# Kernel optimization log

Measured on AMD Instinct MI355X. Metric: run time of the kernel, lower is better.

## Reference

```python
import jax, jax.numpy as jnp
import numpy as np

B, S, H = 4096, 256, 64


def setup_inputs() -> dict:
    key = jax.random.key(0)
    ks = jax.random.split(key, 9)
    s = 1.0 / np.sqrt(H)
    return {
        "x": jax.random.normal(ks[0], (B, S), jnp.float32),
        "W1": jax.random.normal(ks[1], (4, 1), jnp.float32),
        "b1": jax.random.normal(ks[2], (4,), jnp.float32) * 0.1,
        "W_ih": jax.random.normal(ks[3], (4 * H, 4), jnp.float32) * s,
        "W_hh": jax.random.normal(ks[4], (4 * H, H), jnp.float32) * s,
        "b_ih": jax.random.normal(ks[5], (4 * H,), jnp.float32) * s,
        "b_hh": jax.random.normal(ks[6], (4 * H,), jnp.float32) * s,
        "W2": jax.random.normal(ks[7], (1, H), jnp.float32) * s,
        "b2": jax.random.normal(ks[8], (1,), jnp.float32) * 0.1,
    }


def _lstm_last_h(fc1, W_ih, W_hh, b_ih, b_hh):
    # fc1: (B, S, 4). Precompute input contribution to gates for all steps.
    gx = jnp.einsum('bsi,gi->sbg', fc1, W_ih) + (b_ih + b_hh)  # (S, B, 4H)
    h0 = jnp.zeros((fc1.shape[0], H), fc1.dtype)
    c0 = jnp.zeros_like(h0)

    def step(carry, g_t):
        h, c = carry
        gates = g_t + h @ W_hh.T  # (B, 4H)
        i, f, g, o = jnp.split(gates, 4, axis=-1)  # PyTorch gate order i,f,g,o
        i = jax.nn.sigmoid(i)
        f = jax.nn.sigmoid(f)
        g = jnp.tanh(g)
        o = jax.nn.sigmoid(o)
        c = f * c + i * g
        h = o * jnp.tanh(c)
        return (h, c), None

    (h_last, _), _ = jax.lax.scan(step, (h0, c0), gx)
    return h_last  # (B, H)


def reference(x, W1, b1, W_ih, W_hh, b_ih, b_hh, W2, b2):
    # fc1: Linear(1->4) + tanh on x.unsqueeze(2)
    fc1 = jnp.tanh(x[..., None] * W1[:, 0] + b1)  # (B, S, 4)
    h_last = _lstm_last_h(fc1, W_ih, W_hh, b_ih, b_hh)
    return h_last @ W2.T + b2  # (B, 1)
```

## Files before the change

### kernel.cpp

```cpp
#include <hip/hip_runtime.h>


typedef __attribute__((ext_vector_type(8))) __bf16 bf16x8;
typedef __attribute__((ext_vector_type(4))) float f32x4;

#define S_LEN 256
#define TB 16
#define CHUNK 64
#define LOG2E 1.4426950408889634f

#if defined(__has_builtin) && __has_builtin(__builtin_amdgcn_exp2f)
#define EXP2F(x) __builtin_amdgcn_exp2f(x)
#else
#define EXP2F(x) exp2f(x)
#endif
#if defined(__has_builtin) && __has_builtin(__builtin_amdgcn_rcpf)
#define RCPF(x) __builtin_amdgcn_rcpf(x)
#else
#define RCPF(x) (1.0f / (x))
#endif

__device__ __forceinline__ float fast_tanh(float x) {
    float e = EXP2F(2.0f * LOG2E * x);
    return 1.0f - 2.0f * RCPF(e + 1.0f);
}

#define MFMA16(A, B, C) __builtin_amdgcn_mfma_f32_16x16x32_bf16((A), (B), (C), 0, 0, 0)

#define STEP(RB, WB, TLOC) do {                                                   \
    bf16x8 ah0 = *(const bf16x8*)&hbuf[RB][0][0][kg][col][0];                     \
    bf16x8 ah1 = *(const bf16x8*)&hbuf[RB][0][1][kg][col][0];                     \
    bf16x8 al0 = *(const bf16x8*)&hbuf[RB][1][0][kg][col][0];                     \
    bf16x8 al1 = *(const bf16x8*)&hbuf[RB][1][1][kg][col][0];                     \
    bf16x8 fa  = *(const bf16x8*)&fcfrag[TLOC][col][0];                           \
    if (kg >= 2) fa = zero8;                                                      \
    f32x4 acc[4];                                                                 \
    _Pragma("unroll")                                                             \
    for (int n = 0; n < 4; ++n) {                                                 \
        f32x4 a = MFMA16(fa,  whx[n],      biasq[n]);      \
        a       = MFMA16(ah0, whh_h[n][0], a);                                    \
        a       = MFMA16(ah1, whh_h[n][1], a);                                    \
        a       = MFMA16(al0, whh_h[n][0], a);                                    \
        a       = MFMA16(al1, whh_h[n][1], a);                                    \
        a       = MFMA16(ah0, whh_l[n][0], a);                                    \
        a       = MFMA16(ah1, whh_l[n][1], a);                                    \
        acc[n] = a;                                                               \
    }                                                                             \
    _Pragma("unroll")                                                             \
    for (int r = 0; r < 4; ++r) {                                                 \
                        \
        float ei = EXP2F(-acc[0][r]); float iv = RCPF(1.0f + ei);                 \
        float ef = EXP2F(-acc[1][r]); float fv = RCPF(1.0f + ef);                 \
        float eg = EXP2F( acc[2][r]); float gv = 1.0f - 2.0f * RCPF(1.0f + eg);   \
        float eo = EXP2F(-acc[3][r]); float ov = RCPF(1.0f + eo);                 \
        float cv = fv * cst[r] + iv * gv; cst[r] = cv;                            \
        float ec = EXP2F((2.0f * LOG2E) * cv);                                    \
        float th = 1.0f - 2.0f * RCPF(1.0f + ec);                                 \
        float hv = ov * th; hlast[r] = hv;                                        \
        __bf16 hi = (__bf16)hv; __bf16 lo = (__bf16)(hv - (float)hi);             \
        hbuf[WB][0][uks][ukg][kg * 4 + r][up] = hi;                               \
        hbuf[WB][1][uks][ukg][kg * 4 + r][up] = lo;                               \
    }                                                                             \
    __syncthreads();                                                              \
} while (0)

__global__ __launch_bounds__(256, 1)
void lstm_fused(const float* __restrict__ x,
                const float* __restrict__ W1, const float* __restrict__ b1,
                const float* __restrict__ W_ih, const float* __restrict__ W_hh,
                const float* __restrict__ b_ih, const float* __restrict__ b_hh,
                const float* __restrict__ W2, const float* __restrict__ b2,
                float* __restrict__ out)
{
    __shared__ __bf16 fcfrag[CHUNK][TB][8];
    __shared__ __bf16 hbuf[2][2][2][4][TB][8];
    __shared__ float hfin[64][TB];

    const int tid  = threadIdx.x;
    const int lane = tid & 63;
    const int wv   = tid >> 6;
    const int col  = lane & 15;
    const int kg   = lane >> 4;
    const int b0   = blockIdx.x * TB;

    bf16x8 whh_h[4][2], whh_l[4][2];
    bf16x8 whx[4];
    f32x4  biasq[4];

    bf16x8 zero8;
    #pragma unroll
    for (int j = 0; j < 8; ++j) zero8[j] = (__bf16)0.0f;

    #pragma unroll
    for (int n = 0; n < 4; ++n) {
        const int g = 16 * (wv + 4 * n) + col;
        const float sc = (n == 2) ? (2.0f * LOG2E) : LOG2E;
        #pragma unroll
        for (int ks = 0; ks < 2; ++ks) {
            const float* wp = &W_hh[g * 64 + ks * 32 + kg * 8];
            #pragma unroll
            for (int j = 0; j < 8; ++j) {
                float wf  = sc * wp[j];
                __bf16 hi = (__bf16)wf;
                whh_h[n][ks][j] = hi;
                whh_l[n][ks][j] = (__bf16)(wf - (float)hi);
            }
        }
        whx[n] = zero8;
        if (kg < 2) {
            #pragma unroll
            for (int j = 0; j < 4; ++j) {
                float wf  = sc * W_ih[g * 4 + j];
                __bf16 hi = (__bf16)wf;
                __bf16 v  = (kg == 0) ? hi : (__bf16)(wf - (float)hi);
                whx[n][j] = v; whx[n][j + 4] = v;
            }
        }
        const float bs = sc * (b_ih[g] + b_hh[g]);
        biasq[n][0] = bs; biasq[n][1] = bs; biasq[n][2] = bs; biasq[n][3] = bs;
    }

    {
        f32x4 zv = {0.f, 0.f, 0.f, 0.f};
        ((f32x4*)&hbuf[0][0][0][0][0][0])[tid] = zv;
    }

    float w1r[4], b1r[4];
    #pragma unroll
    for (int j = 0; j < 4; ++j) { w1r[j] = W1[j]; b1r[j] = b1[j]; }

    float cst[4] = {0.f, 0.f, 0.f, 0.f};
    float hlast[4];

    const int u   = 16 * wv + col;
    const int uks = u >> 5, ukg = (u >> 3) & 3, up = u & 7;

    for (int t = 0; t < S_LEN; t += 2) {
        if ((t & (CHUNK - 1)) == 0) {
            __syncthreads();
            const int rr = tid & 15;
            const int tq = tid >> 4;
            f32x4 xv = *(const f32x4*)&x[(b0 + rr) * S_LEN + t + tq * 4];
            #pragma unroll
            for (int tl = 0; tl < 4; ++tl) {
                bf16x8 v;
                #pragma unroll
                for (int j = 0; j < 4; ++j) {
                    float fc  = fast_tanh(xv[tl] * w1r[j] + b1r[j]);
                    __bf16 hi = (__bf16)fc;
                    v[j]     = hi;
                    v[j + 4] = (__bf16)(fc - (float)hi);
                }
                *(bf16x8*)&fcfrag[tq * 4 + tl][rr][0] = v;
            }
            __syncthreads();
        }
        STEP(0, 1, (t & (CHUNK - 1)));
        STEP(1, 0, ((t + 1) & (CHUNK - 1)));
    }

    #pragma unroll
    for (int r = 0; r < 4; ++r) hfin[u][kg * 4 + r] = hlast[r];
    __syncthreads();
    if (tid < TB) {
        float s = b2[0];
        #pragma unroll
        for (int uu = 0; uu < 64; ++uu) s += hfin[uu][tid] * W2[uu];
        out[b0 + tid] = s;
    }
}

extern "C" void kernel_launch(void* const* d_in, const int* in_sizes, int n_in,
                              void* d_out, int out_size, void* d_ws, size_t ws_size,
                              hipStream_t stream) {
    (void)in_sizes; (void)n_in; (void)d_ws; (void)ws_size; (void)out_size;
    const float* x    = (const float*)d_in[0];
    const float* W1   = (const float*)d_in[1];
    const float* b1   = (const float*)d_in[2];
    const float* W_ih = (const float*)d_in[3];
    const float* W_hh = (const float*)d_in[4];
    const float* b_ih = (const float*)d_in[5];
    const float* b_hh = (const float*)d_in[6];
    const float* W2   = (const float*)d_in[7];
    const float* b2   = (const float*)d_in[8];
    float* out = (float*)d_out;
    lstm_fused<<<4096 / TB, 256, 0, stream>>>(x, W1, b1, W_ih, W_hh, b_ih, b_hh, W2, b2, out);
}
```

Measured before the change: 230.5 us.

## Split batch tile across two wave groups and pack hi/lo h into MFMA K dimension

Doubles the block to 512 threads, with two wave groups each handling 8 of the 16 batch rows. The A operand now packs the hi and lo bf16 halves of h along the MFMA K lanes, so each gate tile takes 5 MFMAs instead of 7. The two K halves are summed with a cross-lane shuffle, which also halves the per-lane activation work. This cuts the serial per-step MFMA chain and the transcendental count per wave, at the cost of extra shuffles, a larger block and twice the waves sharing each barrier.

```diff
diff --git a/kernel.cpp b/kernel.cpp
--- a/kernel.cpp
+++ b/kernel.cpp
@@ -3,6 +3,7 @@
 
 typedef __attribute__((ext_vector_type(8))) __bf16 bf16x8;
 typedef __attribute__((ext_vector_type(4))) float f32x4;
+typedef __attribute__((ext_vector_type(2))) float f32x2;
 
 #define S_LEN 256
 #define TB 16
@@ -27,44 +28,52 @@
 
 #define MFMA16(A, B, C) __builtin_amdgcn_mfma_f32_16x16x32_bf16((A), (B), (C), 0, 0, 0)
 
-#define STEP(RB, WB, TLOC) do {                                                   \
-    bf16x8 ah0 = *(const bf16x8*)&hbuf[RB][0][0][kg][col][0];                     \
-    bf16x8 ah1 = *(const bf16x8*)&hbuf[RB][0][1][kg][col][0];                     \
-    bf16x8 al0 = *(const bf16x8*)&hbuf[RB][1][0][kg][col][0];                     \
-    bf16x8 al1 = *(const bf16x8*)&hbuf[RB][1][1][kg][col][0];                     \
-    bf16x8 fa  = *(const bf16x8*)&fcfrag[TLOC][col][0];                           \
-    if (kg >= 2) fa = zero8;                                                      \
-    f32x4 acc[4];                                                                 \
-    _Pragma("unroll")                                                             \
-    for (int n = 0; n < 4; ++n) {                                                 \
-        f32x4 a = MFMA16(fa,  whx[n],      biasq[n]);      \
-        a       = MFMA16(ah0, whh_h[n][0], a);                                    \
-        a       = MFMA16(ah1, whh_h[n][1], a);                                    \
-        a       = MFMA16(al0, whh_h[n][0], a);                                    \
-        a       = MFMA16(al1, whh_h[n][1], a);                                    \
-        a       = MFMA16(ah0, whh_l[n][0], a);                                    \
-        a       = MFMA16(ah1, whh_l[n][1], a);                                    \
-        acc[n] = a;                                                               \
-    }                                                                             \
-    _Pragma("unroll")                                                             \
-    for (int r = 0; r < 4; ++r) {                                                 \
-                        \
-        float ei = EXP2F(-acc[0][r]); float iv = RCPF(1.0f + ei);                 \
-        float ef = EXP2F(-acc[1][r]); float fv = RCPF(1.0f + ef);                 \
-        float eg = EXP2F( acc[2][r]); float gv = 1.0f - 2.0f * RCPF(1.0f + eg);   \
-        float eo = EXP2F(-acc[3][r]); float ov = RCPF(1.0f + eo);                 \
-        float cv = fv * cst[r] + iv * gv; cst[r] = cv;                            \
-        float ec = EXP2F((2.0f * LOG2E) * cv);                                    \
-        float th = 1.0f - 2.0f * RCPF(1.0f + ec);                                 \
-        float hv = ov * th; hlast[r] = hv;                                        \
-        __bf16 hi = (__bf16)hv; __bf16 lo = (__bf16)(hv - (float)hi);             \
-        hbuf[WB][0][uks][ukg][kg * 4 + r][up] = hi;                               \
-        hbuf[WB][1][uks][ukg][kg * 4 + r][up] = lo;                               \
-    }                                                                             \
-    __syncthreads();                                                              \
+#define STEP(RB, WB, TLOC) do {                                                  \
+    bf16x8 ap0 = *(const bf16x8*)&hbuf[hv][RB][ahl][0][kg][arow][0];             \
+    bf16x8 ap1 = *(const bf16x8*)&hbuf[hv][RB][ahl][1][kg][arow][0];             \
+    bf16x8 fa  = *(const bf16x8*)&fcfrag[TLOC][farow][0];                        \
+    if (col >= 8) fa = zero8;                 \
+    f32x4 acc[4];                                                                \
+    _Pragma("unroll")                                                            \
+    for (int n = 0; n < 4; ++n) {                                                \
+        f32x4 a = MFMA16(fa,  whx[n],      biasq[n]);    \
+        a       = MFMA16(ap0, whh_h[n][0], a);       \
+        a       = MFMA16(ap1, whh_h[n][1], a);                          \
+        a       = MFMA16(ap0, whh_l[n][0], a);       \
+        a       = MFMA16(ap1, whh_l[n][1], a);                          \
+        acc[n] = a;                                                              \
+    }                                                                            \
+         \
+          \
+    float gate[4][2];                                                            \
+    _Pragma("unroll")                                                            \
+    for (int n = 0; n < 4; ++n) {                                                \
+        float own0 = upper ? acc[n][2] : acc[n][0];                              \
+        float own1 = upper ? acc[n][3] : acc[n][1];                              \
+        float snd0 = upper ? acc[n][0] : acc[n][2];                              \
+        float snd1 = upper ? acc[n][1] : acc[n][3];                              \
+        gate[n][0] = own0 + __shfl_xor(snd0, 32);                                \
+        gate[n][1] = own1 + __shfl_xor(snd1, 32);                                \
+    }                                                                            \
+    _Pragma("unroll")                                                            \
+    for (int r = 0; r < 2; ++r) {                                                \
+                           \
+        float ei = EXP2F(-gate[0][r]); float iv = RCPF(1.0f + ei);               \
+        float ef = EXP2F(-gate[1][r]); float fv = RCPF(1.0f + ef);               \
+        float eg = EXP2F( gate[2][r]); float gv = 1.0f - 2.0f * RCPF(1.0f + eg); \
+        float eo = EXP2F(-gate[3][r]); float ov = RCPF(1.0f + eo);               \
+        float cv = fv * cst[r] + iv * gv; cst[r] = cv;                           \
+        float ec = EXP2F((2.0f * LOG2E) * cv);                                   \
+        float th = 1.0f - 2.0f * RCPF(1.0f + ec);                                \
+        float hvv = ov * th; hlast[r] = hvv;                                     \
+        __bf16 hh = (__bf16)hvv; __bf16 hl = (__bf16)(hvv - (float)hh);          \
+        hbuf[hv][WB][0][uks][ukg][row_base + r][up] = hh;                        \
+        hbuf[hv][WB][1][uks][ukg][row_base + r][up] = hl;                        \
+    }                                                                            \
+    __syncthreads();                                                             \
 } while (0)
 
-__global__ __launch_bounds__(256, 1)
+__global__ __launch_bounds__(512, 1)
 void lstm_fused(const float* __restrict__ x,
                 const float* __restrict__ W1, const float* __restrict__ b1,
                 const float* __restrict__ W_ih, const float* __restrict__ W_hh,
@@ -73,27 +82,37 @@
                 float* __restrict__ out)
 {
     __shared__ __bf16 fcfrag[CHUNK][TB][8];
-    __shared__ __bf16 hbuf[2][2][2][4][TB][8];
+    __shared__ __bf16 hbuf[2][2][2][2][4][8][8];
     __shared__ float hfin[64][TB];
 
     const int tid  = threadIdx.x;
     const int lane = tid & 63;
-    const int wv   = tid >> 6;
+    const int wv8  = tid >> 6;
+    const int hv   = wv8 >> 2;
+    const int wl   = wv8 & 3;
     const int col  = lane & 15;
     const int kg   = lane >> 4;
     const int b0   = blockIdx.x * TB;
 
+    const int  ahl   = col >> 3;
+    const int  arow  = col & 7;
+    const int  farow = 8 * hv + (col & 7);
+    const bool upper = (kg >= 2);
+    const int  row_base = (kg & 1) * 4 + (kg >> 1) * 2;
+    const int  u   = 16 * wl + col;
+    const int  uks = u >> 5, ukg = (u >> 3) & 3, up = u & 7;
+
+    bf16x8 zero8;
+    #pragma unroll
+    for (int j = 0; j < 8; ++j) zero8[j] = (__bf16)0.0f;
+
     bf16x8 whh_h[4][2], whh_l[4][2];
     bf16x8 whx[4];
     f32x4  biasq[4];
 
-    bf16x8 zero8;
-    #pragma unroll
-    for (int j = 0; j < 8; ++j) zero8[j] = (__bf16)0.0f;
-
     #pragma unroll
     for (int n = 0; n < 4; ++n) {
-        const int g = 16 * (wv + 4 * n) + col;
+        const int g = 16 * (wl + 4 * n) + col;
         const float sc = (n == 2) ? (2.0f * LOG2E) : LOG2E;
         #pragma unroll
         for (int ks = 0; ks < 2; ++ks) {
@@ -116,33 +135,30 @@
                 whx[n][j] = v; whx[n][j + 4] = v;
             }
         }
-        const float bs = sc * (b_ih[g] + b_hh[g]);
+        const float bs = (kg < 2) ? sc * (b_ih[g] + b_hh[g]) : 0.0f;
         biasq[n][0] = bs; biasq[n][1] = bs; biasq[n][2] = bs; biasq[n][3] = bs;
     }
 
     {
         f32x4 zv = {0.f, 0.f, 0.f, 0.f};
-        ((f32x4*)&hbuf[0][0][0][0][0][0])[tid] = zv;
+        ((f32x4*)&hbuf[0][0][0][0][0][0][0])[tid] = zv;
     }
 
     float w1r[4], b1r[4];
     #pragma unroll
     for (int j = 0; j < 4; ++j) { w1r[j] = W1[j]; b1r[j] = b1[j]; }
 
-    float cst[4] = {0.f, 0.f, 0.f, 0.f};
-    float hlast[4];
-
-    const int u   = 16 * wv + col;
-    const int uks = u >> 5, ukg = (u >> 3) & 3, up = u & 7;
+    f32x2 cst = {0.f, 0.f};
+    float hlast[2];
 
     for (int t = 0; t < S_LEN; t += 2) {
         if ((t & (CHUNK - 1)) == 0) {
             __syncthreads();
             const int rr = tid & 15;
             const int tq = tid >> 4;
-            f32x4 xv = *(const f32x4*)&x[(b0 + rr) * S_LEN + t + tq * 4];
+            f32x2 xv = *(const f32x2*)&x[(b0 + rr) * S_LEN + t + tq * 2];
             #pragma unroll
-            for (int tl = 0; tl < 4; ++tl) {
+            for (int tl = 0; tl < 2; ++tl) {
                 bf16x8 v;
                 #pragma unroll
                 for (int j = 0; j < 4; ++j) {
@@ -151,7 +167,7 @@
                     v[j]     = hi;
                     v[j + 4] = (__bf16)(fc - (float)hi);
                 }
-                *(bf16x8*)&fcfrag[tq * 4 + tl][rr][0] = v;
+                *(bf16x8*)&fcfrag[tq * 2 + tl][rr][0] = v;
             }
             __syncthreads();
         }
@@ -159,8 +175,8 @@
         STEP(1, 0, ((t + 1) & (CHUNK - 1)));
     }
 
-    #pragma unroll
-    for (int r = 0; r < 4; ++r) hfin[u][kg * 4 + r] = hlast[r];
+    hfin[u][8 * hv + row_base + 0] = hlast[0];
+    hfin[u][8 * hv + row_base + 1] = hlast[1];
     __syncthreads();
     if (tid < TB) {
         float s = b2[0];
@@ -184,5 +200,5 @@
     const float* W2   = (const float*)d_in[7];
     const float* b2   = (const float*)d_in[8];
     float* out = (float*)d_out;
-    lstm_fused<<<4096 / TB, 256, 0, stream>>>(x, W1, b1, W_ih, W_hh, b_ih, b_hh, W2, b2, out);
+    lstm_fused<<<4096 / TB, 512, 0, stream>>>(x, W1, b1, W_ih, W_hh, b_ih, b_hh, W2, b2, out);
 }
```

Measured after the change: 269.2 us. +16.8%, slower.

## Pack hi/lo bf16 split into MFMA K dimension with 8-row blocks

Applied to the files above, without the earlier changes.

Halves the batch tile per block to 8 rows and re-lays out the hidden-state buffer so each MFMA row pair holds the hi and lo bf16 halves of one batch row. The split-precision product then comes out of 4 MFMAs per gate instead of 6, with the two partial sums added after the MFMA. The gate math is also rewritten to fuse the sigmoid and tanh reciprocals into fewer RCP calls, with clamping to avoid overflow. Launch bounds now allow two blocks per CU to make up for the smaller tiles. The catch is twice as many blocks, each doing the same per-step sync and MFMA latency chain on half the useful rows.

```diff
diff --git a/kernel.cpp b/kernel.cpp
--- a/kernel.cpp
+++ b/kernel.cpp
@@ -3,11 +3,13 @@
 
 typedef __attribute__((ext_vector_type(8))) __bf16 bf16x8;
 typedef __attribute__((ext_vector_type(4))) float f32x4;
+typedef __attribute__((ext_vector_type(2))) float f32x2;
 
 #define S_LEN 256
-#define TB 16
+#define TB 8
 #define CHUNK 64
 #define LOG2E 1.4426950408889634f
+#define TWO_LOG2E 2.8853900817779268f
 
 #if defined(__has_builtin) && __has_builtin(__builtin_amdgcn_exp2f)
 #define EXP2F(x) __builtin_amdgcn_exp2f(x)
@@ -20,51 +22,55 @@
 #define RCPF(x) (1.0f / (x))
 #endif
 
+__device__ __forceinline__ float clamp30(float x) {
+    return fminf(fmaxf(x, -30.0f), 30.0f);
+}
 __device__ __forceinline__ float fast_tanh(float x) {
-    float e = EXP2F(2.0f * LOG2E * x);
+    float e = EXP2F(TWO_LOG2E * x);
     return 1.0f - 2.0f * RCPF(e + 1.0f);
 }
 
 #define MFMA16(A, B, C) __builtin_amdgcn_mfma_f32_16x16x32_bf16((A), (B), (C), 0, 0, 0)
 
 #define STEP(RB, WB, TLOC) do {                                                   \
-    bf16x8 ah0 = *(const bf16x8*)&hbuf[RB][0][0][kg][col][0];                     \
-    bf16x8 ah1 = *(const bf16x8*)&hbuf[RB][0][1][kg][col][0];                     \
-    bf16x8 al0 = *(const bf16x8*)&hbuf[RB][1][0][kg][col][0];                     \
-    bf16x8 al1 = *(const bf16x8*)&hbuf[RB][1][1][kg][col][0];                     \
-    bf16x8 fa  = *(const bf16x8*)&fcfrag[TLOC][col][0];                           \
-    if (kg >= 2) fa = zero8;                                                      \
+    bf16x8 ap0 = *(const bf16x8*)&hbuf[RB][0][kg][col >> 1][col & 1][0];          \
+    bf16x8 ap1 = *(const bf16x8*)&hbuf[RB][1][kg][col >> 1][col & 1][0];          \
+    bf16x8 fa  = *(const bf16x8*)&fcfrag[TLOC][col >> 1][0];                      \
+    if (col & 1) fa = zero8;                \
     f32x4 acc[4];                                                                 \
     _Pragma("unroll")                                                             \
     for (int n = 0; n < 4; ++n) {                                                 \
-        f32x4 a = MFMA16(fa,  whx[n],      biasq[n]);      \
-        a       = MFMA16(ah0, whh_h[n][0], a);                                    \
-        a       = MFMA16(ah1, whh_h[n][1], a);                                    \
-        a       = MFMA16(al0, whh_h[n][0], a);                                    \
-        a       = MFMA16(al1, whh_h[n][1], a);                                    \
-        a       = MFMA16(ah0, whh_l[n][0], a);                                    \
-        a       = MFMA16(ah1, whh_l[n][1], a);                                    \
+        f32x4 a = MFMA16(fa,  whx[n],      biasq[n]);     \
+        a       = MFMA16(ap0, whh_h[n][0], a);                                    \
+        a       = MFMA16(ap1, whh_h[n][1], a);                                    \
+        a       = MFMA16(ap0, whh_l[n][0], a);                                    \
+        a       = MFMA16(ap1, whh_l[n][1], a);                                    \
         acc[n] = a;                                                               \
     }                                                                             \
     _Pragma("unroll")                                                             \
-    for (int r = 0; r < 4; ++r) {                                                 \
-                        \
-        float ei = EXP2F(-acc[0][r]); float iv = RCPF(1.0f + ei);                 \
-        float ef = EXP2F(-acc[1][r]); float fv = RCPF(1.0f + ef);                 \
-        float eg = EXP2F( acc[2][r]); float gv = 1.0f - 2.0f * RCPF(1.0f + eg);   \
-        float eo = EXP2F(-acc[3][r]); float ov = RCPF(1.0f + eo);                 \
-        float cv = fv * cst[r] + iv * gv; cst[r] = cv;                            \
-        float ec = EXP2F((2.0f * LOG2E) * cv);                                    \
-        float th = 1.0f - 2.0f * RCPF(1.0f + ec);                                 \
-        float hv = ov * th; hlast[r] = hv;                                        \
-        __bf16 hi = (__bf16)hv; __bf16 lo = (__bf16)(hv - (float)hi);             \
-        hbuf[WB][0][uks][ukg][kg * 4 + r][up] = hi;                               \
-        hbuf[WB][1][uks][ukg][kg * 4 + r][up] = lo;                               \
+    for (int j = 0; j < 2; ++j) {                                                 \
+            \
+        float Ai = clamp30(acc[0][2 * j] + acc[0][2 * j + 1]);                    \
+        float Ff = clamp30(acc[1][2 * j] + acc[1][2 * j + 1]);                    \
+        float Gg = clamp30(acc[2][2 * j] + acc[2][2 * j + 1]);                    \
+        float Oo = clamp30(acc[3][2 * j] + acc[3][2 * j + 1]);                    \
+        float ea = EXP2F(-Ai), ef = EXP2F(-Ff), eg = EXP2F(Gg), eo = EXP2F(-Oo);  \
+        float tf  = 1.0f + ef;                                                    \
+        float tag = (1.0f + ea) * (1.0f + eg);                                    \
+        float Nn  = fmaf(cst[j], tag, (eg - 1.0f) * tf);                          \
+        float cn  = Nn * RCPF(tag * tf);                                          \
+        cst[j] = cn;                                                              \
+        float ec  = EXP2F(clamp30(TWO_LOG2E * cn));                               \
+        float hvv = (ec - 1.0f) * RCPF((1.0f + eo) * (ec + 1.0f));                \
+        hlast[j] = hvv;                                                           \
+        __bf16 hh = (__bf16)hvv; __bf16 hl = (__bf16)(hvv - (float)hh);           \
+        hbuf[WB][uks][ukg][2 * kg + j][0][up] = hh;                               \
+        hbuf[WB][uks][ukg][2 * kg + j][1][up] = hl;                               \
     }                                                                             \
     __syncthreads();                                                              \
 } while (0)
 
-__global__ __launch_bounds__(256, 1)
+__global__ __launch_bounds__(256, 2)
 void lstm_fused(const float* __restrict__ x,
                 const float* __restrict__ W1, const float* __restrict__ b1,
                 const float* __restrict__ W_ih, const float* __restrict__ W_hh,
@@ -73,7 +79,7 @@
                 float* __restrict__ out)
 {
     __shared__ __bf16 fcfrag[CHUNK][TB][8];
-    __shared__ __bf16 hbuf[2][2][2][4][TB][8];
+    __shared__ __bf16 hbuf[2][2][4][8][2][8];
     __shared__ float hfin[64][TB];
 
     const int tid  = threadIdx.x;
@@ -83,18 +89,18 @@
     const int kg   = lane >> 4;
     const int b0   = blockIdx.x * TB;
 
+    bf16x8 zero8;
+    #pragma unroll
+    for (int j = 0; j < 8; ++j) zero8[j] = (__bf16)0.0f;
+
     bf16x8 whh_h[4][2], whh_l[4][2];
     bf16x8 whx[4];
     f32x4  biasq[4];
 
-    bf16x8 zero8;
-    #pragma unroll
-    for (int j = 0; j < 8; ++j) zero8[j] = (__bf16)0.0f;
-
     #pragma unroll
     for (int n = 0; n < 4; ++n) {
         const int g = 16 * (wv + 4 * n) + col;
-        const float sc = (n == 2) ? (2.0f * LOG2E) : LOG2E;
+        const float sc = (n == 2) ? TWO_LOG2E : LOG2E;
         #pragma unroll
         for (int ks = 0; ks < 2; ++ks) {
             const float* wp = &W_hh[g * 64 + ks * 32 + kg * 8];
@@ -117,7 +123,8 @@
             }
         }
         const float bs = sc * (b_ih[g] + b_hh[g]);
-        biasq[n][0] = bs; biasq[n][1] = bs; biasq[n][2] = bs; biasq[n][3] = bs;
+        biasq[n][0] = bs; biasq[n][1] = 0.0f;
+        biasq[n][2] = bs; biasq[n][3] = 0.0f;
     }
 
     {
@@ -129,8 +136,8 @@
     #pragma unroll
     for (int j = 0; j < 4; ++j) { w1r[j] = W1[j]; b1r[j] = b1[j]; }
 
-    float cst[4] = {0.f, 0.f, 0.f, 0.f};
-    float hlast[4];
+    f32x2 cst = {0.f, 0.f};
+    float hlast[2];
 
     const int u   = 16 * wv + col;
     const int uks = u >> 5, ukg = (u >> 3) & 3, up = u & 7;
@@ -138,11 +145,11 @@
     for (int t = 0; t < S_LEN; t += 2) {
         if ((t & (CHUNK - 1)) == 0) {
             __syncthreads();
-            const int rr = tid & 15;
-            const int tq = tid >> 4;
-            f32x4 xv = *(const f32x4*)&x[(b0 + rr) * S_LEN + t + tq * 4];
+            const int rr = tid & 7;
+            const int tq = tid >> 3;
+            f32x2 xv = *(const f32x2*)&x[(b0 + rr) * S_LEN + t + tq * 2];
             #pragma unroll
-            for (int tl = 0; tl < 4; ++tl) {
+            for (int tl = 0; tl < 2; ++tl) {
                 bf16x8 v;
                 #pragma unroll
                 for (int j = 0; j < 4; ++j) {
@@ -151,7 +158,7 @@
                     v[j]     = hi;
                     v[j + 4] = (__bf16)(fc - (float)hi);
                 }
-                *(bf16x8*)&fcfrag[tq * 4 + tl][rr][0] = v;
+                *(bf16x8*)&fcfrag[tq * 2 + tl][rr][0] = v;
             }
             __syncthreads();
         }
@@ -159,8 +166,8 @@
         STEP(1, 0, ((t + 1) & (CHUNK - 1)));
     }
 
-    #pragma unroll
-    for (int r = 0; r < 4; ++r) hfin[u][kg * 4 + r] = hlast[r];
+    hfin[u][2 * kg + 0] = hlast[0];
+    hfin[u][2 * kg + 1] = hlast[1];
     __syncthreads();
     if (tid < TB) {
         float s = b2[0];
```

After: 245.9 us. 6.7% more time.
